# Kernel optimization log

Measured on AMD Instinct MI355X. Metric: run time of the kernel, lower is better.

## Reference

```python
import jax, jax.numpy as jnp
import numpy as np

B, W, F, N = 256, 512, 512, 512


def setup_inputs() -> dict:
    key = jax.random.key(0)
    k1, k2, k3, k4, k5 = jax.random.split(key, 5)
    return {
        "x": jax.random.normal(k1, (B, W, F), dtype=jnp.float32),
        "weight_k": jax.random.normal(k2, (F, N), dtype=jnp.float32),
        "weight_q": jax.random.normal(k3, (F, N), dtype=jnp.float32),
        "weight_v": jax.random.normal(k4, (F, N), dtype=jnp.float32),
        "w": jax.random.normal(k5, (W, 1), dtype=jnp.float32),
    }


def reference(x, weight_k, weight_q, weight_v, w):
    # x: (B, W, F)
    n_outputs = weight_k.shape[-1]
    # Per-word K/V projections (original loops over words; here one batched GEMM)
    K = jnp.einsum("bwf,fn->bwn", x, weight_k)  # (B, W, N)
    V = jnp.einsum("bwf,fn->bwn", x, weight_v)  # (B, W, N)
    # Per-sample query: t = x^T @ w -> (F,), q = t @ weight_q -> (N,)
    t = jnp.einsum("bwf,w->bf", x, w[:, 0])     # (B, F)
    Q = t @ weight_q                              # (B, N)
    # Scores over words, scaled, softmax across the word axis
    scores = jnp.einsum("bn,bwn->bw", Q, K) / jnp.sqrt(jnp.float32(n_outputs))
    weights = jax.nn.softmax(scores, axis=1)      # (B, W)
    # Weighted sum of V over words
    return jnp.einsum("bw,bwn->bn", weights, V)   # (B, N)
```

## Files before the change

kernel.cpp:

```cpp
#include <hip/hip_runtime.h>
#include <math.h>

#define B 256
#define W 512
#define F 512
#define N 512

__global__ __launch_bounds__(512) void fused_attn_kernel(
    const float* __restrict__ x,
    const float* __restrict__ Wq,
    const float* __restrict__ Wk,
    const float* __restrict__ Wv,
    const float* __restrict__ wvec,
    float* __restrict__ out)
{
    const int b    = blockIdx.x;
    const int tid  = threadIdx.x;
    const int lane = tid & 63;
    const int wv   = tid >> 6;

    __shared__ float s_w[W];
    __shared__ float s_c[8][F];
    __shared__ float s_t[F];
    __shared__ float s_q[N];
    __shared__ float s_r[F];
    __shared__ float s_m[8];
    __shared__ float s_l[8];
    __shared__ float s_cf[F];

    const float* xb = x + (size_t)b * W * F;

    s_w[tid] = wvec[tid];
    __syncthreads();

    {
        float4 t0 = make_float4(0.f, 0.f, 0.f, 0.f);
        float4 t1 = make_float4(0.f, 0.f, 0.f, 0.f);
#pragma unroll 2
        for (int i = 0; i < 64; i += 4) {
            const float* row = xb + (size_t)(wv * 64 + i) * F;
            float4 a0[4], a1[4];
#pragma unroll
            for (int j = 0; j < 4; ++j) {
                a0[j] = *(const float4*)(row + (size_t)j * F + lane * 4);
                a1[j] = *(const float4*)(row + (size_t)j * F + 256 + lane * 4);
            }
#pragma unroll
            for (int j = 0; j < 4; ++j) {
                const float ww = s_w[wv * 64 + i + j];
                t0.x += a0[j].x * ww; t0.y += a0[j].y * ww;
                t0.z += a0[j].z * ww; t0.w += a0[j].w * ww;
                t1.x += a1[j].x * ww; t1.y += a1[j].y * ww;
                t1.z += a1[j].z * ww; t1.w += a1[j].w * ww;
            }
        }
        *(float4*)&s_c[wv][lane * 4]       = t0;
        *(float4*)&s_c[wv][256 + lane * 4] = t1;
    }
    __syncthreads();

    {
        float t = 0.f;
#pragma unroll
        for (int j = 0; j < 8; ++j) t += s_c[j][tid];
        s_t[tid] = t;
    }
    __syncthreads();

    {
        float q0 = 0.f, q1 = 0.f, q2 = 0.f, q3 = 0.f;
#pragma unroll 4
        for (int f = 0; f < F; f += 4) {
            q0 += s_t[f + 0] * Wq[(size_t)(f + 0) * N + tid];
            q1 += s_t[f + 1] * Wq[(size_t)(f + 1) * N + tid];
            q2 += s_t[f + 2] * Wq[(size_t)(f + 2) * N + tid];
            q3 += s_t[f + 3] * Wq[(size_t)(f + 3) * N + tid];
        }
        s_q[tid] = (q0 + q1) + (q2 + q3);
    }
    __syncthreads();

    {
        const float4* wkrow = (const float4*)(Wk + (size_t)tid * N);
        float r0 = 0.f, r1 = 0.f, r2 = 0.f, r3 = 0.f;
#pragma unroll 8
        for (int n4 = 0; n4 < N / 4; ++n4) {
            const float4 kv = wkrow[n4];
            const float4 qv = *(const float4*)&s_q[n4 * 4];
            r0 += kv.x * qv.x; r1 += kv.y * qv.y;
            r2 += kv.z * qv.z; r3 += kv.w * qv.w;
        }
        s_r[tid] = ((r0 + r1) + (r2 + r3)) * 0.04419417382415922f;
    }
    __syncthreads();

    const float4 r0 = *(const float4*)&s_r[lane * 4];
    const float4 r1 = *(const float4*)&s_r[256 + lane * 4];

    float m = -INFINITY, l = 0.f;
    float4 c0 = make_float4(0.f, 0.f, 0.f, 0.f);
    float4 c1 = make_float4(0.f, 0.f, 0.f, 0.f);

#pragma unroll 2
    for (int t = 0; t < 8; ++t) {
        const float* row = xb + (size_t)(wv * 64 + t * 8) * F;

        float4 xa0[8], xa1[8];
#pragma unroll
        for (int j = 0; j < 8; ++j) {
            xa0[j] = *(const float4*)(row + (size_t)j * F + lane * 4);
            xa1[j] = *(const float4*)(row + (size_t)j * F + 256 + lane * 4);
        }

        float d[8];
#pragma unroll
        for (int j = 0; j < 8; ++j) {
            d[j] = xa0[j].x * r0.x + xa0[j].y * r0.y
                 + xa0[j].z * r0.z + xa0[j].w * r0.w
                 + xa1[j].x * r1.x + xa1[j].y * r1.y
                 + xa1[j].z * r1.z + xa1[j].w * r1.w;
        }

#pragma unroll
        for (int off = 32; off >= 1; off >>= 1) {
#pragma unroll
            for (int j = 0; j < 8; ++j)
                d[j] += __shfl_xor(d[j], off, 64);
        }

        const float mb = fmaxf(fmaxf(fmaxf(d[0], d[1]), fmaxf(d[2], d[3])),
                               fmaxf(fmaxf(d[4], d[5]), fmaxf(d[6], d[7])));
        const float mn = fmaxf(m, mb);
        const float sc = __expf(m - mn);

        float p[8];
        float ps = 0.f;
#pragma unroll
        for (int j = 0; j < 8; ++j) {
            p[j] = __expf(d[j] - mn);
            ps += p[j];
        }
        l = l * sc + ps;

        float ax = c0.x * sc, ay = c0.y * sc, az = c0.z * sc, aw = c0.w * sc;
#pragma unroll
        for (int j = 0; j < 8; ++j) {
            ax += p[j] * xa0[j].x; ay += p[j] * xa0[j].y;
            az += p[j] * xa0[j].z; aw += p[j] * xa0[j].w;
        }
        c0 = make_float4(ax, ay, az, aw);

        ax = c1.x * sc; ay = c1.y * sc; az = c1.z * sc; aw = c1.w * sc;
#pragma unroll
        for (int j = 0; j < 8; ++j) {
            ax += p[j] * xa1[j].x; ay += p[j] * xa1[j].y;
            az += p[j] * xa1[j].z; aw += p[j] * xa1[j].w;
        }
        c1 = make_float4(ax, ay, az, aw);

        m = mn;
    }

    __syncthreads();
    *(float4*)&s_c[wv][lane * 4]       = c0;
    *(float4*)&s_c[wv][256 + lane * 4] = c1;
    if (lane == 0) { s_m[wv] = m; s_l[wv] = l; }
    __syncthreads();

    float M = -INFINITY;
#pragma unroll
    for (int j = 0; j < 8; ++j) M = fmaxf(M, s_m[j]);
    float L = 0.f;
    float alpha[8];
#pragma unroll
    for (int j = 0; j < 8; ++j) {
        alpha[j] = __expf(s_m[j] - M);
        L += alpha[j] * s_l[j];
    }
    const float invL = 1.f / L;

    float cf = 0.f;
#pragma unroll
    for (int j = 0; j < 8; ++j) cf += alpha[j] * s_c[j][tid];
    s_cf[tid] = cf * invL;
    __syncthreads();

    float o0 = 0.f, o1 = 0.f, o2 = 0.f, o3 = 0.f;
#pragma unroll 4
    for (int f = 0; f < F; f += 4) {
        o0 += s_cf[f + 0] * Wv[(size_t)(f + 0) * N + tid];
        o1 += s_cf[f + 1] * Wv[(size_t)(f + 1) * N + tid];
        o2 += s_cf[f + 2] * Wv[(size_t)(f + 2) * N + tid];
        o3 += s_cf[f + 3] * Wv[(size_t)(f + 3) * N + tid];
    }
    out[(size_t)b * N + tid] = (o0 + o1) + (o2 + o3);
}

extern "C" void kernel_launch(void* const* d_in, const int* in_sizes, int n_in,
                              void* d_out, int out_size, void* d_ws, size_t ws_size,
                              hipStream_t stream)
{
    const float* x    = (const float*)d_in[0];
    const float* Wk   = (const float*)d_in[1];
    const float* Wq   = (const float*)d_in[2];
    const float* Wv   = (const float*)d_in[3];
    const float* wvec = (const float*)d_in[4];
    float* out = (float*)d_out;

    fused_attn_kernel<<<B, 512, 0, stream>>>(x, Wq, Wk, Wv, wvec, out);
}
```

Baseline: 455.0 us.

## Double block size to 16 waves and split projections across two halves

Launches 1024 threads per block instead of 512, so each wave covers 32 words instead of 64 in both the t-reduction and online-softmax passes. The Wq, Wk and Wv matvecs are split along the reduction dimension between two 512-thread halves, with partial sums combined through a new shared buffer. The aim is to give each CU more waves in flight to hide memory latency on the large per-sample x stream. The cost is extra shared-memory round trips and barriers, plus a 16-way merge of the online-softmax state, and register pressure is capped by the larger block.

```diff
diff --git a/kernel.cpp b/kernel.cpp
--- a/kernel.cpp
+++ b/kernel.cpp
@@ -5,8 +5,9 @@
 #define W 512
 #define F 512
 #define N 512
-
-__global__ __launch_bounds__(512) void fused_attn_kernel(
+#define NWAVE 16
+
+__global__ __launch_bounds__(1024, 4) void fused_attn_kernel(
     const float* __restrict__ x,
     const float* __restrict__ Wq,
     const float* __restrict__ Wk,
@@ -18,36 +19,39 @@
     const int tid  = threadIdx.x;
     const int lane = tid & 63;
     const int wv   = tid >> 6;
+    const int f5   = tid & 511;
+    const int half = tid >> 9;
 
     __shared__ float s_w[W];
-    __shared__ float s_c[8][F];
+    __shared__ float s_c[NWAVE][F];
+    __shared__ float s_p2[2][F];
     __shared__ float s_t[F];
     __shared__ float s_q[N];
     __shared__ float s_r[F];
-    __shared__ float s_m[8];
-    __shared__ float s_l[8];
+    __shared__ float s_m[NWAVE];
+    __shared__ float s_l[NWAVE];
     __shared__ float s_cf[F];
 
     const float* xb = x + (size_t)b * W * F;
 
-    s_w[tid] = wvec[tid];
+    if (tid < W) s_w[tid] = wvec[tid];
     __syncthreads();
 
     {
         float4 t0 = make_float4(0.f, 0.f, 0.f, 0.f);
         float4 t1 = make_float4(0.f, 0.f, 0.f, 0.f);
+        const float* base = xb + (size_t)(wv * 32) * F;
 #pragma unroll 2
-        for (int i = 0; i < 64; i += 4) {
-            const float* row = xb + (size_t)(wv * 64 + i) * F;
+        for (int i = 0; i < 32; i += 4) {
             float4 a0[4], a1[4];
 #pragma unroll
             for (int j = 0; j < 4; ++j) {
-                a0[j] = *(const float4*)(row + (size_t)j * F + lane * 4);
-                a1[j] = *(const float4*)(row + (size_t)j * F + 256 + lane * 4);
+                a0[j] = *(const float4*)(base + (size_t)(i + j) * F + lane * 4);
+                a1[j] = *(const float4*)(base + (size_t)(i + j) * F + 256 + lane * 4);
             }
 #pragma unroll
             for (int j = 0; j < 4; ++j) {
-                const float ww = s_w[wv * 64 + i + j];
+                const float ww = s_w[wv * 32 + i + j];
                 t0.x += a0[j].x * ww; t0.y += a0[j].y * ww;
                 t0.z += a0[j].z * ww; t0.w += a0[j].w * ww;
                 t1.x += a1[j].x * ww; t1.y += a1[j].y * ww;
@@ -60,38 +64,46 @@
     __syncthreads();
 
     {
-        float t = 0.f;
-#pragma unroll
-        for (int j = 0; j < 8; ++j) t += s_c[j][tid];
-        s_t[tid] = t;
-    }
-    __syncthreads();
-
-    {
+        float tp = 0.f;
+#pragma unroll
+        for (int j = 0; j < 8; ++j) tp += s_c[half * 8 + j][f5];
+        s_p2[half][f5] = tp;
+    }
+    __syncthreads();
+    if (tid < F) s_t[tid] = s_p2[0][tid] + s_p2[1][tid];
+    __syncthreads();
+
+    {
+        const int fb = half * 256;
         float q0 = 0.f, q1 = 0.f, q2 = 0.f, q3 = 0.f;
 #pragma unroll 4
-        for (int f = 0; f < F; f += 4) {
-            q0 += s_t[f + 0] * Wq[(size_t)(f + 0) * N + tid];
-            q1 += s_t[f + 1] * Wq[(size_t)(f + 1) * N + tid];
-            q2 += s_t[f + 2] * Wq[(size_t)(f + 2) * N + tid];
-            q3 += s_t[f + 3] * Wq[(size_t)(f + 3) * N + tid];
-        }
-        s_q[tid] = (q0 + q1) + (q2 + q3);
-    }
-    __syncthreads();
-
-    {
-        const float4* wkrow = (const float4*)(Wk + (size_t)tid * N);
+        for (int f = 0; f < 256; f += 4) {
+            q0 += s_t[fb + f + 0] * Wq[(size_t)(fb + f + 0) * N + f5];
+            q1 += s_t[fb + f + 1] * Wq[(size_t)(fb + f + 1) * N + f5];
+            q2 += s_t[fb + f + 2] * Wq[(size_t)(fb + f + 2) * N + f5];
+            q3 += s_t[fb + f + 3] * Wq[(size_t)(fb + f + 3) * N + f5];
+        }
+        s_p2[half][f5] = (q0 + q1) + (q2 + q3);
+    }
+    __syncthreads();
+    if (tid < N) s_q[tid] = s_p2[0][tid] + s_p2[1][tid];
+    __syncthreads();
+
+    {
+        const float4* wkrow = (const float4*)(Wk + (size_t)f5 * N + half * 256);
+        const float4* qv4   = (const float4*)&s_q[half * 256];
         float r0 = 0.f, r1 = 0.f, r2 = 0.f, r3 = 0.f;
 #pragma unroll 8
-        for (int n4 = 0; n4 < N / 4; ++n4) {
+        for (int n4 = 0; n4 < 64; ++n4) {
             const float4 kv = wkrow[n4];
-            const float4 qv = *(const float4*)&s_q[n4 * 4];
-            r0 += kv.x * qv.x; r1 += kv.y * qv.y;
-            r2 += kv.z * qv.z; r3 += kv.w * qv.w;
-        }
-        s_r[tid] = ((r0 + r1) + (r2 + r3)) * 0.04419417382415922f;
-    }
+            const float4 qq = qv4[n4];
+            r0 += kv.x * qq.x; r1 += kv.y * qq.y;
+            r2 += kv.z * qq.z; r3 += kv.w * qq.w;
+        }
+        s_p2[half][f5] = (r0 + r1) + (r2 + r3);
+    }
+    __syncthreads();
+    if (tid < F) s_r[tid] = (s_p2[0][tid] + s_p2[1][tid]) * 0.04419417382415922f;
     __syncthreads();
 
     const float4 r0 = *(const float4*)&s_r[lane * 4];
@@ -102,8 +114,8 @@
     float4 c1 = make_float4(0.f, 0.f, 0.f, 0.f);
 
 #pragma unroll 2
-    for (int t = 0; t < 8; ++t) {
-        const float* row = xb + (size_t)(wv * 64 + t * 8) * F;
+    for (int t = 0; t < 4; ++t) {
+        const float* row = xb + (size_t)(wv * 32 + t * 8) * F;
 
         float4 xa0[8], xa1[8];
 #pragma unroll
@@ -161,7 +173,6 @@
         m = mn;
     }
 
-    __syncthreads();
     *(float4*)&s_c[wv][lane * 4]       = c0;
     *(float4*)&s_c[wv][256 + lane * 4] = c1;
     if (lane == 0) { s_m[wv] = m; s_l[wv] = l; }
@@ -169,31 +180,40 @@
 
     float M = -INFINITY;
 #pragma unroll
-    for (int j = 0; j < 8; ++j) M = fmaxf(M, s_m[j]);
+    for (int j = 0; j < NWAVE; ++j) M = fmaxf(M, s_m[j]);
     float L = 0.f;
-    float alpha[8];
-#pragma unroll
-    for (int j = 0; j < 8; ++j) {
+    float alpha[NWAVE];
+#pragma unroll
+    for (int j = 0; j < NWAVE; ++j) {
         alpha[j] = __expf(s_m[j] - M);
         L += alpha[j] * s_l[j];
     }
     const float invL = 1.f / L;
 
-    float cf = 0.f;
-#pragma unroll
-    for (int j = 0; j < 8; ++j) cf += alpha[j] * s_c[j][tid];
-    s_cf[tid] = cf * invL;
-    __syncthreads();
-
-    float o0 = 0.f, o1 = 0.f, o2 = 0.f, o3 = 0.f;
+    {
+        float cp = 0.f;
+#pragma unroll
+        for (int j = 0; j < 8; ++j) cp += alpha[half * 8 + j] * s_c[half * 8 + j][f5];
+        s_p2[half][f5] = cp;
+    }
+    __syncthreads();
+    if (tid < F) s_cf[tid] = (s_p2[0][tid] + s_p2[1][tid]) * invL;
+    __syncthreads();
+
+    {
+        const int fb = half * 256;
+        float o0 = 0.f, o1 = 0.f, o2 = 0.f, o3 = 0.f;
 #pragma unroll 4
-    for (int f = 0; f < F; f += 4) {
-        o0 += s_cf[f + 0] * Wv[(size_t)(f + 0) * N + tid];
-        o1 += s_cf[f + 1] * Wv[(size_t)(f + 1) * N + tid];
-        o2 += s_cf[f + 2] * Wv[(size_t)(f + 2) * N + tid];
-        o3 += s_cf[f + 3] * Wv[(size_t)(f + 3) * N + tid];
-    }
-    out[(size_t)b * N + tid] = (o0 + o1) + (o2 + o3);
+        for (int f = 0; f < 256; f += 4) {
+            o0 += s_cf[fb + f + 0] * Wv[(size_t)(fb + f + 0) * N + f5];
+            o1 += s_cf[fb + f + 1] * Wv[(size_t)(fb + f + 1) * N + f5];
+            o2 += s_cf[fb + f + 2] * Wv[(size_t)(fb + f + 2) * N + f5];
+            o3 += s_cf[fb + f + 3] * Wv[(size_t)(fb + f + 3) * N + f5];
+        }
+        s_p2[half][f5] = (o0 + o1) + (o2 + o3);
+    }
+    __syncthreads();
+    if (tid < N) out[(size_t)b * N + tid] = s_p2[0][tid] + s_p2[1][tid];
 }
 
 extern "C" void kernel_launch(void* const* d_in, const int* in_sizes, int n_in,
@@ -207,5 +227,5 @@
     const float* wvec = (const float*)d_in[4];
     float* out = (float*)d_out;
 
-    fused_attn_kernel<<<B, 512, 0, stream>>>(x, Wq, Wk, Wv, wvec, out);
+    fused_attn_kernel<<<B, 1024, 0, stream>>>(x, Wq, Wk, Wv, wvec, out);
 }
```

Result: no change. 448.4 us (-1.5%).
